# Kernel optimization log

Measured on AMD Instinct MI355X. Metric: run time of the kernel, lower is better.

The kernel has to match this reference:

```python
import jax, jax.numpy as jnp
import numpy as np

PATCH_SIZE = 3  # init kwarg; kernels are 1x1 so this only sets conv padding
PAD = PATCH_SIZE // 2


def setup_inputs() -> dict:
    key = jax.random.key(0)
    k1, k2 = jax.random.split(key)
    foreground = jax.random.normal(k1, (4, 256, 64, 64), dtype=jnp.float32)
    mask = jax.random.uniform(k2, (4, 1, 64, 64), dtype=jnp.float32)
    return {"foreground": foreground, "mask": mask}


def reference(foreground, mask):
    # foreground: [bs, ch, h, w]; mask: [bs, 1, h, w]
    bs, ch, h, w = foreground.shape
    hw = h * w
    p = PAD

    # per-pixel 1x1 conv kernels: [bs, hw, ch], +1e-7 then L2-normalize over ch
    K = jnp.transpose(foreground.reshape(bs, ch, hw), (0, 2, 1)) + 1e-7
    Kn = K / jnp.sqrt(jnp.sum(K * K, axis=2, keepdims=True))

    # conv2d with 1x1 kernels and padding p == matmul against zero-padded map
    Fp = jnp.pad(foreground, ((0, 0), (0, 0), (p, p), (p, p)))  # [bs, ch, h+2p, w+2p]
    scores = jnp.einsum('bjc,bcyx->bjyx', Kn, Fp)  # [bs, hw, h+2p, w+2p]
    att = jax.nn.softmax(scores, axis=1)

    # mask-weighted kernels, then conv_transpose2d (1x1, padding p) == matmul + crop
    m_flat = mask[:, 0].reshape(bs, hw)  # [bs, hw]
    Km = Kn * m_flat[:, :, None]
    out_pad = jnp.einsum('bjc,bjyx->bcyx', Km, att)  # [bs, ch, h+2p, w+2p]
    fmap_mask = out_pad[:, :, p:p + h, p:p + w]  # crop padding -> [bs, ch, h, w]

    mm = mask[:, 0:1]  # [bs, 1, h, w]
    final = fmap_mask * (1.0 - mm) + foreground * mm

    # skip branch: nearly-all-ones mask passes the feature map through unchanged
    skip = jnp.sum(mm, axis=(1, 2, 3)) > (h * w - 10)  # [bs]
    return jnp.where(skip[:, None, None, None], foreground, final)
```

## Files before the change

kernel.cpp:

```cpp
#include <hip/hip_runtime.h>
#include <hip/hip_bf16.h>
#include <math.h>

typedef __bf16 bf16x8 __attribute__((ext_vector_type(8)));
typedef float  f32x4  __attribute__((ext_vector_type(4)));
typedef unsigned int u32;

#define BS 4
#define CH 256
#define HW 4096
#define QB 64
#define KB 64
#define NKT (HW/KB)
#define NQT (HW/QB)
#define LOG2E 1.44269504f

__device__ __host__ inline int uperm(int jl) {
  return ((jl & 15) << 2) | (((jl >> 5) & 1) << 1) | ((jl >> 4) & 1);
}

__global__ __launch_bounds__(256) void prep_kernel(
    const float* __restrict__ F, const float* __restrict__ mask,
    __bf16* __restrict__ Kn, __bf16* __restrict__ Kmt2, float* __restrict__ norms)
{
  __shared__ float tile[256 * 33];
  __shared__ float red[256];
  __shared__ float invs[32];
  __shared__ float mld[32];
  const int t  = threadIdx.x;
  const int b  = blockIdx.y;
  const int j0 = blockIdx.x * 32;

  {
    const int jj = t & 31, cr = t >> 5;
    for (int it = 0; it < 32; ++it) {
      int c = it * 8 + cr;
      tile[c * 33 + jj] = F[(size_t)(b * CH + c) * HW + j0 + jj];
    }
  }
  if (t < 32) mld[t] = mask[b * HW + j0 + t];
  __syncthreads();

  {
    const int jj = t & 31, part = t >> 5;
    float s = 0.f;
    for (int c = part * 32; c < part * 32 + 32; ++c) {
      float v = tile[c * 33 + jj] + 1e-7f;
      s += v * v;
    }
    red[part * 32 + jj] = s;
  }
  __syncthreads();
  if (t < 32) {
    float s = 0.f;
    for (int p = 0; p < 8; ++p) s += red[p * 32 + t];
    invs[t] = rsqrtf(s);
    norms[b * HW + j0 + t] = sqrtf(s) * LOG2E;
  }
  __syncthreads();

  for (int jj = 0; jj < 32; ++jj) {
    float v  = tile[t * 33 + jj];
    float kn = (v + 1e-7f) * invs[jj];
    Kn[(size_t)(b * HW + j0 + jj) * CH + t] = (__bf16)kn;
    tile[t * 33 + jj] = kn * mld[jj];
  }
  __syncthreads();

  {
    const int jj = t & 31, cr = t >> 5;
    for (int it = 0; it < 32; ++it) {
      int c = it * 8 + cr;
      int j = j0 + jj;
      int t64 = j >> 6, jl = j & 63;
      Kmt2[(((size_t)(b * NKT + t64)) * CH + c) * 64 + uperm(jl)] = (__bf16)tile[c * 33 + jj];
    }
  }
}

__global__ __launch_bounds__(256) void skip_kernel(
    const float* __restrict__ mask, float* __restrict__ flags)
{
  __shared__ float wsum[4];
  const int b = blockIdx.x, t = threadIdx.x;
  float s = 0.f;
  for (int i = t; i < HW; i += 256) s += mask[b * HW + i];
  for (int off = 32; off; off >>= 1) s += __shfl_down(s, off);
  if ((t & 63) == 0) wsum[t >> 6] = s;
  __syncthreads();
  if (t == 0) {
    float tot = wsum[0] + wsum[1] + wsum[2] + wsum[3];
    flags[b] = (tot > (float)(HW - 10)) ? 1.f : 0.f;
  }
}

__device__ inline u32 pkbf(float a, float b) {
  union { __bf16 h[2]; u32 u; } cv;
  cv.h[0] = (__bf16)a; cv.h[1] = (__bf16)b;
  return cv.u;
}

__global__ __launch_bounds__(512, 2) void attn_kernel(
    const __bf16* __restrict__ Kn, const __bf16* __restrict__ Kmt2,
    const float* __restrict__ norms,
    __bf16* __restrict__ Opart, float* __restrict__ lhalf, int jn)
{
  __shared__ __align__(16) __bf16 Ks[64 * 256];
  __shared__ __align__(16) __bf16 Ps[64 * 72];
  char* KsB = (char*)Ks;
  char* PsB = (char*)Ps;

  const int t = threadIdx.x;
  const int w = t >> 6, lane = t & 63, lg = lane >> 4, lr = lane & 15;
  const int g = w >> 1, jh = w & 1;
  const int l5 = lane >> 5;

  const int bid = blockIdx.x;
  const int nc  = 4 * jn;
  int combo, qt;
  if (nc == 8) { combo = bid & 7; qt = bid >> 3; }
  else         { combo = bid % nc; qt = bid / nc; }
  const int b   = combo / jn, js = combo % jn;
  const int KT  = NKT / jn;
  const int kt0 = js * KT;
  const int q0  = qt * QB;

  const int cb = (lane & 31) * 16;

  bf16x8 qf[8];
  {
    const __bf16* qrow = Kn + (size_t)(b * HW + q0 + g * 16 + lr) * CH;
    #pragma unroll
    for (int ks = 0; ks < 8; ++ks)
      qf[ks] = *(const bf16x8*)(qrow + ks * 32 + lg * 8);
  }
  float nrm[4];
  #pragma unroll
  for (int r = 0; r < 4; ++r)
    nrm[r] = norms[b * HW + q0 + g * 16 + lg * 4 + r];

  f32x4 acc[2][4];
  #pragma unroll
  for (int i = 0; i < 2; ++i)
    #pragma unroll
    for (int j = 0; j < 4; ++j) acc[i][j] = (f32x4)0.f;
  float l_part[4];
  #pragma unroll
  for (int r = 0; r < 4; ++r) l_part[r] = 0.f;

  #pragma unroll
  for (int i = 0; i < 4; ++i) {
    const int rr = i * 16 + w * 2 + l5;
    const char* gsrc = (const char*)(Kn + (size_t)(b * HW + kt0 * KB + rr) * CH) +
                       (cb ^ ((rr & 7) << 4));
    char* ldst = KsB + (i * 16 + w * 2) * 512;
    __builtin_amdgcn_global_load_lds(
        (const __attribute__((address_space(1))) u32*)gsrc,
        (__attribute__((address_space(3))) u32*)ldst, 16, 0, 0);
  }
  __syncthreads();

  for (int k = 0; k < KT; ++k) {
    const int kt = kt0 + k;

    f32x4 sa[2];
    #pragma unroll
    for (int n = 0; n < 2; ++n) sa[n] = (f32x4)0.f;
    __builtin_amdgcn_s_setprio(1);
    #pragma unroll
    for (int ks = 0; ks < 8; ++ks) {
      bf16x8 bb[2];
      #pragma unroll
      for (int n = 0; n < 2; ++n) {
        const int row = jh * 32 + n * 16 + lr;
        bb[n] = *(const bf16x8*)(KsB + row * 512 + ((ks * 64 + lg * 16) ^ ((row & 7) << 4)));
      }
      #pragma unroll
      for (int n = 0; n < 2; ++n)
        sa[n] = __builtin_amdgcn_mfma_f32_16x16x32_bf16(qf[ks], bb[n], sa[n], 0, 0, 0);
    }
    __builtin_amdgcn_s_setprio(0);

    #pragma unroll
    for (int r = 0; r < 4; ++r) {
      float e0 = exp2f(sa[0][r] * nrm[r]);
      float e1 = exp2f(sa[1][r] * nrm[r]);
      l_part[r] += e0 + e1;
      const int q = g * 16 + lg * 4 + r;
      *(u32*)(PsB + q * 144 + 8 * lr + 4 * jh) = pkbf(e0, e1);
    }
    __syncthreads();

    if (k + 1 < KT) {
      #pragma unroll
      for (int i = 0; i < 4; ++i) {
        const int rr = i * 16 + w * 2 + l5;
        const char* gsrc = (const char*)(Kn + (size_t)(b * HW + (kt + 1) * KB + rr) * CH) +
                           (cb ^ ((rr & 7) << 4));
        char* ldst = KsB + (i * 16 + w * 2) * 512;
        __builtin_amdgcn_global_load_lds(
            (const __attribute__((address_space(1))) u32*)gsrc,
            (__attribute__((address_space(3))) u32*)ldst, 16, 0, 0);
      }
    }

    __builtin_amdgcn_s_setprio(1);
    #pragma unroll
    for (int ks2 = 0; ks2 < 2; ++ks2) {
      bf16x8 pfr[4], km[2];
      #pragma unroll
      for (int nt = 0; nt < 4; ++nt)
        pfr[nt] = *(const bf16x8*)(PsB + (nt * 16 + lr) * 144 + ks2 * 64 + lg * 16);
      #pragma unroll
      for (int mt = 0; mt < 2; ++mt)
        km[mt] = *(const bf16x8*)(Kmt2 + (((size_t)(b * NKT + kt)) * CH + 32 * w + mt * 16 + lr) * 64 +
                                  ks2 * 32 + lg * 8);
      #pragma unroll
      for (int mt = 0; mt < 2; ++mt)
        #pragma unroll
        for (int nt = 0; nt < 4; ++nt)
          acc[mt][nt] = __builtin_amdgcn_mfma_f32_16x16x32_bf16(km[mt], pfr[nt], acc[mt][nt], 0, 0, 0);
    }
    __builtin_amdgcn_s_setprio(0);
    __syncthreads();
  }

  __bf16* op = Opart + ((size_t)(js * BS + b) * NQT + qt) * QB * CH;
  #pragma unroll
  for (int mt = 0; mt < 2; ++mt) {
    const int cbn = 32 * w + mt * 16 + lg * 4;
    #pragma unroll
    for (int nt = 0; nt < 4; ++nt) {
      const int q = nt * 16 + lr;
      uint2 pw2;
      pw2.x = pkbf(acc[mt][nt][0], acc[mt][nt][1]);
      pw2.y = pkbf(acc[mt][nt][2], acc[mt][nt][3]);
      *(uint2*)(op + (size_t)q * CH + cbn) = pw2;
    }
  }
  #pragma unroll
  for (int r = 0; r < 4; ++r) {
    float v = l_part[r];
    v += __shfl_xor(v, 1); v += __shfl_xor(v, 2);
    v += __shfl_xor(v, 4); v += __shfl_xor(v, 8);
    l_part[r] = v;
  }
  if (lr == 0) {
    #pragma unroll
    for (int r = 0; r < 4; ++r) {
      int qg = q0 + g * 16 + lg * 4 + r;
      lhalf[((size_t)(js * 2 + jh) * BS + b) * HW + qg] = l_part[r];
    }
  }
}

__global__ __launch_bounds__(256) void combine_kernel(
    const __bf16* __restrict__ Opart, const float* __restrict__ lhalf,
    const float* __restrict__ F, const float* __restrict__ mask,
    const float* __restrict__ flags, float* __restrict__ out, int jn)
{
  const int bid = blockIdx.x;
  const int cq = bid & 3, chunk = bid >> 2;
  const int t = threadIdx.x;
  const int qg = chunk * 256 + t;
  const int b  = qg >> 12, q = qg & 4095;
  const int qt = q >> 6, ql = q & 63;

  float L = 0.f;
  for (int s = 0; s < 2 * jn; ++s)
    L += lhalf[((size_t)s * BS + b) * HW + q];
  float inv = 1.f / L;
  float msk = mask[b * HW + q];
  float w1 = 1.f - msk;
  bool skip = flags[b] > 0.5f;

  const __bf16* opq[4];
  for (int js = 0; js < jn; ++js)
    opq[js] = Opart + (((size_t)(js * BS + b) * NQT + qt) * QB + ql) * CH;

  for (int c0 = cq * 64; c0 < cq * 64 + 64; c0 += 8) {
    float s8[8];
    #pragma unroll
    for (int e = 0; e < 8; ++e) s8[e] = 0.f;
    for (int js = 0; js < jn; ++js) {
      bf16x8 v = *(const bf16x8*)(opq[js] + c0);
      #pragma unroll
      for (int e = 0; e < 8; ++e) s8[e] += (float)v[e];
    }
    #pragma unroll
    for (int e = 0; e < 8; ++e) {
      size_t idx = ((size_t)b * CH + c0 + e) * HW + q;
      float f = F[idx];
      out[idx] = skip ? f : (s8[e] * inv * w1 + f * msk);
    }
  }
}

extern "C" void kernel_launch(void* const* d_in, const int* in_sizes, int n_in,
                              void* d_out, int out_size, void* d_ws, size_t ws_size,
                              hipStream_t stream) {
  const float* F    = (const float*)d_in[0];
  const float* mask = (const float*)d_in[1];
  float* out = (float*)d_out;

  char* p = (char*)d_ws;
  __bf16* Kn   = (__bf16*)p;  p += (size_t)BS * HW * CH * 2;
  __bf16* Kmt2 = (__bf16*)p;  p += (size_t)BS * HW * CH * 2;
  float* norms = (float*)p;   p += (size_t)BS * HW * 4;
  float* flags = (float*)p;   p += 256;
  size_t used = (size_t)(p - (char*)d_ws);

  int jn = 2;
  while (jn > 1) {
    size_t need = used + (size_t)jn * ((size_t)2 * BS * HW * 4 + (size_t)BS * NQT * QB * CH * 2);
    if (need <= ws_size) break;
    jn >>= 1;
  }
  float* lh = (float*)p;      p += (size_t)2 * jn * BS * HW * 4;
  __bf16* Opart = (__bf16*)p;

  prep_kernel<<<dim3(HW / 32, BS), 256, 0, stream>>>(F, mask, Kn, Kmt2, norms);
  skip_kernel<<<BS, 256, 0, stream>>>(mask, flags);
  attn_kernel<<<dim3(NQT * 4 * jn), 512, 0, stream>>>(Kn, Kmt2, norms, Opart, lh, jn);
  combine_kernel<<<dim3(256), 256, 0, stream>>>(Opart, lh, F, mask, flags, out, jn);
}
```

Before: 180.6 us.

## Remap attention waves to share key fragments across two query tiles and raise occupancy

Each wave now owns 32 query rows (two MFMA M-tiles) and a 16-key quarter of the key tile instead of 16 queries and 32 keys. One LDS key fragment load now feeds two MFMAs, and the row-sum partials are split four ways, so the combine kernel and workspace sizing change to match. The Kmt2 permutation is dropped, which changes how the P*V step reads its layout. Launch bounds are raised to four blocks per multiprocessor, which limits registers while the kernel now holds twice as many Q fragments. The P stores become scalar bf16 writes, which adds LDS store instructions.

```diff
diff --git a/kernel.cpp b/kernel.cpp
--- a/kernel.cpp
+++ b/kernel.cpp
@@ -14,10 +14,6 @@
 #define NKT (HW/KB)
 #define NQT (HW/QB)
 #define LOG2E 1.44269504f
-
-__device__ __host__ inline int uperm(int jl) {
-  return ((jl & 15) << 2) | (((jl >> 5) & 1) << 1) | ((jl >> 4) & 1);
-}
 
 __global__ __launch_bounds__(256) void prep_kernel(
     const float* __restrict__ F, const float* __restrict__ mask,
@@ -73,7 +69,7 @@
       int c = it * 8 + cr;
       int j = j0 + jj;
       int t64 = j >> 6, jl = j & 63;
-      Kmt2[(((size_t)(b * NKT + t64)) * CH + c) * 64 + uperm(jl)] = (__bf16)tile[c * 33 + jj];
+      Kmt2[(((size_t)(b * NKT + t64)) * CH + c) * 64 + jl] = (__bf16)tile[c * 33 + jj];
     }
   }
 }
@@ -100,7 +96,7 @@
   return cv.u;
 }
 
-__global__ __launch_bounds__(512, 2) void attn_kernel(
+__global__ __launch_bounds__(512, 4) void attn_kernel(
     const __bf16* __restrict__ Kn, const __bf16* __restrict__ Kmt2,
     const float* __restrict__ norms,
     __bf16* __restrict__ Opart, float* __restrict__ lhalf, int jn)
@@ -112,7 +108,7 @@
 
   const int t = threadIdx.x;
   const int w = t >> 6, lane = t & 63, lg = lane >> 4, lr = lane & 15;
-  const int g = w >> 1, jh = w & 1;
+  const int g = w & 1, jq = w >> 1;
   const int l5 = lane >> 5;
 
   const int bid = blockIdx.x;
@@ -127,26 +123,31 @@
 
   const int cb = (lane & 31) * 16;
 
-  bf16x8 qf[8];
-  {
-    const __bf16* qrow = Kn + (size_t)(b * HW + q0 + g * 16 + lr) * CH;
+  bf16x8 qf[2][8];
+  #pragma unroll
+  for (int m = 0; m < 2; ++m) {
+    const __bf16* qrow = Kn + (size_t)(b * HW + q0 + g * 32 + m * 16 + lr) * CH;
     #pragma unroll
     for (int ks = 0; ks < 8; ++ks)
-      qf[ks] = *(const bf16x8*)(qrow + ks * 32 + lg * 8);
-  }
-  float nrm[4];
-  #pragma unroll
-  for (int r = 0; r < 4; ++r)
-    nrm[r] = norms[b * HW + q0 + g * 16 + lg * 4 + r];
+      qf[m][ks] = *(const bf16x8*)(qrow + ks * 32 + lg * 8);
+  }
+  float nrm[2][4];
+  #pragma unroll
+  for (int m = 0; m < 2; ++m)
+    #pragma unroll
+    for (int r = 0; r < 4; ++r)
+      nrm[m][r] = norms[b * HW + q0 + g * 32 + m * 16 + lg * 4 + r];
 
   f32x4 acc[2][4];
   #pragma unroll
   for (int i = 0; i < 2; ++i)
     #pragma unroll
     for (int j = 0; j < 4; ++j) acc[i][j] = (f32x4)0.f;
-  float l_part[4];
-  #pragma unroll
-  for (int r = 0; r < 4; ++r) l_part[r] = 0.f;
+  float l_part[2][4];
+  #pragma unroll
+  for (int m = 0; m < 2; ++m)
+    #pragma unroll
+    for (int r = 0; r < 4; ++r) l_part[m][r] = 0.f;
 
   #pragma unroll
   for (int i = 0; i < 4; ++i) {
@@ -165,29 +166,27 @@
 
     f32x4 sa[2];
     #pragma unroll
-    for (int n = 0; n < 2; ++n) sa[n] = (f32x4)0.f;
+    for (int m = 0; m < 2; ++m) sa[m] = (f32x4)0.f;
     __builtin_amdgcn_s_setprio(1);
     #pragma unroll
     for (int ks = 0; ks < 8; ++ks) {
-      bf16x8 bb[2];
-      #pragma unroll
-      for (int n = 0; n < 2; ++n) {
-        const int row = jh * 32 + n * 16 + lr;
-        bb[n] = *(const bf16x8*)(KsB + row * 512 + ((ks * 64 + lg * 16) ^ ((row & 7) << 4)));
+      const int row = jq * 16 + lr;
+      bf16x8 bb = *(const bf16x8*)(KsB + row * 512 + ((ks * 64 + lg * 16) ^ ((row & 7) << 4)));
+      #pragma unroll
+      for (int m = 0; m < 2; ++m)
+        sa[m] = __builtin_amdgcn_mfma_f32_16x16x32_bf16(qf[m][ks], bb, sa[m], 0, 0, 0);
+    }
+    __builtin_amdgcn_s_setprio(0);
+
+    #pragma unroll
+    for (int m = 0; m < 2; ++m) {
+      #pragma unroll
+      for (int r = 0; r < 4; ++r) {
+        float e = exp2f(sa[m][r] * nrm[m][r]);
+        l_part[m][r] += e;
+        const int q = g * 32 + m * 16 + lg * 4 + r;
+        *(__bf16*)(PsB + q * 144 + jq * 32 + 2 * lr) = (__bf16)e;
       }
-      #pragma unroll
-      for (int n = 0; n < 2; ++n)
-        sa[n] = __builtin_amdgcn_mfma_f32_16x16x32_bf16(qf[ks], bb[n], sa[n], 0, 0, 0);
-    }
-    __builtin_amdgcn_s_setprio(0);
-
-    #pragma unroll
-    for (int r = 0; r < 4; ++r) {
-      float e0 = exp2f(sa[0][r] * nrm[r]);
-      float e1 = exp2f(sa[1][r] * nrm[r]);
-      l_part[r] += e0 + e1;
-      const int q = g * 16 + lg * 4 + r;
-      *(u32*)(PsB + q * 144 + 8 * lr + 4 * jh) = pkbf(e0, e1);
     }
     __syncthreads();
 
@@ -239,18 +238,22 @@
     }
   }
   #pragma unroll
-  for (int r = 0; r < 4; ++r) {
-    float v = l_part[r];
-    v += __shfl_xor(v, 1); v += __shfl_xor(v, 2);
-    v += __shfl_xor(v, 4); v += __shfl_xor(v, 8);
-    l_part[r] = v;
-  }
+  for (int m = 0; m < 2; ++m)
+    #pragma unroll
+    for (int r = 0; r < 4; ++r) {
+      float v = l_part[m][r];
+      v += __shfl_xor(v, 1); v += __shfl_xor(v, 2);
+      v += __shfl_xor(v, 4); v += __shfl_xor(v, 8);
+      l_part[m][r] = v;
+    }
   if (lr == 0) {
     #pragma unroll
-    for (int r = 0; r < 4; ++r) {
-      int qg = q0 + g * 16 + lg * 4 + r;
-      lhalf[((size_t)(js * 2 + jh) * BS + b) * HW + qg] = l_part[r];
-    }
+    for (int m = 0; m < 2; ++m)
+      #pragma unroll
+      for (int r = 0; r < 4; ++r) {
+        int qg = q0 + g * 32 + m * 16 + lg * 4 + r;
+        lhalf[((size_t)(js * 4 + jq) * BS + b) * HW + qg] = l_part[m][r];
+      }
   }
 }
 
@@ -267,7 +270,7 @@
   const int qt = q >> 6, ql = q & 63;
 
   float L = 0.f;
-  for (int s = 0; s < 2 * jn; ++s)
+  for (int s = 0; s < 4 * jn; ++s)
     L += lhalf[((size_t)s * BS + b) * HW + q];
   float inv = 1.f / L;
   float msk = mask[b * HW + q];
@@ -312,11 +315,11 @@
 
   int jn = 2;
   while (jn > 1) {
-    size_t need = used + (size_t)jn * ((size_t)2 * BS * HW * 4 + (size_t)BS * NQT * QB * CH * 2);
+    size_t need = used + (size_t)jn * ((size_t)4 * BS * HW * 4 + (size_t)BS * NQT * QB * CH * 2);
     if (need <= ws_size) break;
     jn >>= 1;
   }
-  float* lh = (float*)p;      p += (size_t)2 * jn * BS * HW * 4;
+  float* lh = (float*)p;      p += (size_t)4 * jn * BS * HW * 4;
   __bf16* Opart = (__bf16*)p;
 
   prep_kernel<<<dim3(HW / 32, BS), 256, 0, stream>>>(F, mask, Kn, Kmt2, norms);
```

Result: slower. 326.8 us (+81.0%).
